# Optimization experiments

Hardware: AMD Instinct MI355X
Metric: run time of the kernel (lower is better)

## Reference

```python
import jax, jax.numpy as jnp
import numpy as np

N = 50000
E = 600000
D_IN, D_HID, D_OUT = 128, 128, 64


def gcn_conv(x, edge_index, W, b):
    """PyG GCNConv: add self-loops, symmetric deg^{-1/2} normalization,
    linear transform, scatter-add aggregation, bias."""
    n = x.shape[0]
    loop = jnp.arange(n, dtype=edge_index.dtype)
    src = jnp.concatenate([edge_index[0], loop])
    dst = jnp.concatenate([edge_index[1], loop])
    h = x @ W  # [N, out]
    deg = jax.ops.segment_sum(jnp.ones_like(dst, dtype=h.dtype), dst, num_segments=n)
    dinv = jnp.where(deg > 0, jax.lax.rsqrt(jnp.maximum(deg, 1e-12)), 0.0)
    norm = dinv[src] * dinv[dst]  # [E+N]
    msg = h[src] * norm[:, None]  # gather + scale
    out = jax.ops.segment_sum(msg, dst, num_segments=n)  # scatter-add
    return out + b


def setup_inputs() -> dict:
    key = jax.random.key(0)
    k1, k2, k3, k4 = jax.random.split(key, 4)
    x = jax.random.normal(k1, (N, D_IN), dtype=jnp.float32)
    edge_index = jax.random.randint(k2, (2, E), 0, N, dtype=jnp.int64)
    s1 = (1.0 / np.sqrt(D_IN)).astype(np.float32) if False else np.float32(1.0 / np.sqrt(D_IN))
    s2 = np.float32(1.0 / np.sqrt(D_HID))
    W1 = jax.random.normal(k3, (D_IN, D_HID), dtype=jnp.float32) * s1
    b1 = jnp.zeros((D_HID,), dtype=jnp.float32)
    W2 = jax.random.normal(k4, (D_HID, D_OUT), dtype=jnp.float32) * s2
    b2 = jnp.zeros((D_OUT,), dtype=jnp.float32)
    return {"x": x, "edge_index": edge_index, "W1": W1, "b1": b1, "W2": W2, "b2": b2}


def reference(x, edge_index, W1, b1, W2, b2):
    # eval mode: dropout p = 0
    h = jax.nn.relu(gcn_conv(x, edge_index, W1, b1))
    return gcn_conv(h, edge_index, W2, b2)
```

## Files before the change

kernel.cpp:

```cpp
#include <hip/hip_runtime.h>
#include <hip/hip_fp16.h>
#include <stdint.h>

#define DIN 128
#define DHID 128
#define DOUT2 64

__device__ __forceinline__ unsigned short f2bf(float f) {
    unsigned u = __float_as_uint(f);
    u += 0x7fffu + ((u >> 16) & 1u);
    return (unsigned short)(u >> 16);
}
__device__ __forceinline__ float bf2f(unsigned short b) {
    return __uint_as_float(((unsigned)b) << 16);
}
__device__ __forceinline__ float bflo(unsigned v) { return __uint_as_float(v << 16); }
__device__ __forceinline__ float bfhi(unsigned v) { return __uint_as_float(v & 0xffff0000u); }
__device__ __forceinline__ unsigned short f2h(float f) {
    return __half_as_ushort(__float2half_rn(f));
}
__device__ __forceinline__ float h2f(unsigned bits) {
    return __half2float(__ushort_as_half((unsigned short)bits));
}

__global__ void detect_i64_kernel(const unsigned* ei, int* flag) {
    int t = threadIdx.x;
    unsigned hi = ei[2 * t + 1];
    unsigned long long vote = __ballot(hi == 0u);
    if (t == 0) *flag = (vote == ~0ull) ? 1 : 0;
}

template <int DO, typename AT>
__device__ __forceinline__ void gemm_block(const AT* __restrict__ A, const float* __restrict__ W,
                                           unsigned short* __restrict__ out, int M, int bx,
                                           float* As, float* Bs) {
    constexpr int CG  = DO / 4;
    constexpr int TYN = 256 / CG;
    constexpr int RM  = 64 / TYN;
    const int tid = threadIdx.x;
    const int row0 = bx * 64;
    const int tx = tid % CG, ty = tid / CG;

    float acc[RM][4];
#pragma unroll
    for (int r = 0; r < RM; r++) acc[r][0] = acc[r][1] = acc[r][2] = acc[r][3] = 0.f;

    for (int k0 = 0; k0 < 128; k0 += 64) {
        for (int idx = tid; idx < 64 * 16; idx += 256) {
            int r = idx >> 4, cc = idx & 15;
            int row = row0 + r;
            float4 v = make_float4(0.f, 0.f, 0.f, 0.f);
            if (row < M) {
                if constexpr (sizeof(AT) == 4) {
                    v = ((const float4*)A)[(size_t)row * 32 + (k0 >> 2) + cc];
                } else {
                    ushort4 u = ((const ushort4*)A)[(size_t)row * 32 + (k0 >> 2) + cc];
                    v = make_float4(bf2f(u.x), bf2f(u.y), bf2f(u.z), bf2f(u.w));
                }
            }
            ((float4*)As)[idx] = v;
        }
        for (int idx = tid; idx < 64 * CG; idx += 256) {
            int r = idx / CG, cc = idx % CG;
            ((float4*)Bs)[idx] = ((const float4*)W)[(size_t)(k0 + r) * CG + cc];
        }
        __syncthreads();
#pragma unroll 8
        for (int k = 0; k < 64; k++) {
            float4 b = ((const float4*)Bs)[k * CG + tx];
#pragma unroll
            for (int r = 0; r < RM; r++) {
                float a = As[(ty * RM + r) * 64 + k];
                acc[r][0] = fmaf(a, b.x, acc[r][0]);
                acc[r][1] = fmaf(a, b.y, acc[r][1]);
                acc[r][2] = fmaf(a, b.z, acc[r][2]);
                acc[r][3] = fmaf(a, b.w, acc[r][3]);
            }
        }
        __syncthreads();
    }
#pragma unroll
    for (int r = 0; r < RM; r++) {
        int row = row0 + ty * RM + r;
        if (row < M) {
            ushort4 v;
            v.x = f2bf(acc[r][0]);
            v.y = f2bf(acc[r][1]);
            v.z = f2bf(acc[r][2]);
            v.w = f2bf(acc[r][3]);
            ((ushort4*)out)[(size_t)row * CG + tx] = v;
        }
    }
}

__global__ __launch_bounds__(256, 2) void fused_gemm_deg_kernel(
    const float* __restrict__ A, const float* __restrict__ W, unsigned short* __restrict__ out,
    int M, int gemmBlocks, const int* ei32, const long long* ei64, const int* flag,
    unsigned* deg, int E) {
    __shared__ float As[64 * 64];
    __shared__ float Bs[64 * DHID];
    if ((int)blockIdx.x < gemmBlocks) {
        gemm_block<DHID, float>(A, W, out, M, blockIdx.x, As, Bs);
    } else {
        int e = (blockIdx.x - gemmBlocks) * 256 + threadIdx.x;
        if (e < E) {
            int mode = *flag;
            int d = mode ? (int)ei64[(size_t)E + e] : ei32[(size_t)E + e];
            atomicAdd(&deg[d], 1u);
        }
    }
}

template <int DO, typename AT>
__global__ __launch_bounds__(256, 2) void gemm_kernel(const AT* __restrict__ A,
                                                      const float* __restrict__ W,
                                                      unsigned short* __restrict__ out, int M) {
    __shared__ float As[64 * 64];
    __shared__ float Bs[64 * DO];
    gemm_block<DO, AT>(A, W, out, M, blockIdx.x, As, Bs);
}

__global__ __launch_bounds__(256) void scan_blocksum_kernel(const unsigned* deg, int* bsum,
                                                            float* dinv, int N) {
    __shared__ int s[256];
    int t = threadIdx.x;
    int base = blockIdx.x * 1024 + t * 4;
    int sum = 0;
    if (base + 3 < N) {
        int4 v = *(const int4*)((const int*)deg + base);
        sum = v.x + v.y + v.z + v.w;
        float4 dv;
        dv.x = rsqrtf((float)(v.x + 1));
        dv.y = rsqrtf((float)(v.y + 1));
        dv.z = rsqrtf((float)(v.z + 1));
        dv.w = rsqrtf((float)(v.w + 1));
        *(float4*)(dinv + base) = dv;
    } else {
        for (int j = 0; j < 4; j++)
            if (base + j < N) {
                int d = (int)deg[base + j];
                sum += d;
                dinv[base + j] = rsqrtf((float)(d + 1));
            }
    }
    s[t] = sum;
    __syncthreads();
    for (int off = 128; off > 0; off >>= 1) {
        if (t < off) s[t] += s[t + off];
        __syncthreads();
    }
    if (t == 0) bsum[blockIdx.x] = s[0];
}

__global__ __launch_bounds__(256) void scan_bsum_kernel(int* bsum, int* row_ptr, int nb, int N) {
    __shared__ int s[256];
    int t = threadIdx.x;
    int v = (t < nb) ? bsum[t] : 0;
    s[t] = v;
    __syncthreads();
    for (int off = 1; off < 256; off <<= 1) {
        int u = (t >= off) ? s[t - off] : 0;
        __syncthreads();
        s[t] += u;
        __syncthreads();
    }
    if (t < nb) bsum[t] = s[t] - v;
    if (t == 255) row_ptr[N] = s[255];
}

__global__ __launch_bounds__(256) void scan_write_kernel(const unsigned* deg, const int* bsum,
                                                         int* row_ptr, int* cursor, int N) {
    __shared__ int s[256];
    int t = threadIdx.x;
    int base = blockIdx.x * 1024 + t * 4;
    int d[4];
    int sum = 0;
#pragma unroll
    for (int j = 0; j < 4; j++) {
        int idx = base + j;
        d[j] = (idx < N) ? (int)deg[idx] : 0;
        sum += d[j];
    }
    s[t] = sum;
    __syncthreads();
    for (int off = 1; off < 256; off <<= 1) {
        int u = (t >= off) ? s[t - off] : 0;
        __syncthreads();
        s[t] += u;
        __syncthreads();
    }
    int run = bsum[blockIdx.x] + s[t] - sum;
#pragma unroll
    for (int j = 0; j < 4; j++) {
        int idx = base + j;
        if (idx < N) {
            row_ptr[idx] = run;
            cursor[idx] = run;
            run += d[j];
        }
    }
}

__global__ void scatter_pack32_kernel(const int* ei32, const long long* ei64, const int* flag,
                                      const float* dinv, int* cursor, unsigned* csr, int E) {
    int e = blockIdx.x * blockDim.x + threadIdx.x;
    if (e >= E) return;
    int mode = *flag;
    int s, d;
    if (mode) {
        s = (int)ei64[e];
        d = (int)ei64[(size_t)E + e];
    } else {
        s = ei32[e];
        d = ei32[(size_t)E + e];
    }
    int pos = atomicAdd(&cursor[d], 1);
    csr[pos] = (unsigned)s | ((unsigned)f2h(dinv[s]) << 16);
}

__global__ void scatter_pack64_kernel(const int* ei32, const long long* ei64, const int* flag,
                                      const float* dinv, int* cursor, unsigned long long* csr,
                                      int E) {
    int e = blockIdx.x * blockDim.x + threadIdx.x;
    if (e >= E) return;
    int mode = *flag;
    int s, d;
    if (mode) {
        s = (int)ei64[e];
        d = (int)ei64[(size_t)E + e];
    } else {
        s = ei32[e];
        d = ei32[(size_t)E + e];
    }
    int pos = atomicAdd(&cursor[d], 1);
    csr[pos] = (unsigned long long)(unsigned)s |
               ((unsigned long long)__float_as_uint(dinv[s]) << 32);
}

__device__ __forceinline__ void unpack(unsigned p, int& s, float& w) {
    s = (int)(p & 0xffffu);
    w = h2f(p >> 16);
}
__device__ __forceinline__ void unpack(unsigned long long p, int& s, float& w) {
    s = (int)(unsigned)(p & 0xffffffffu);
    w = __uint_as_float((unsigned)(p >> 32));
}

template <int D, bool RELU, typename OT, typename CT>
__global__ __launch_bounds__(256) void agg_kernel(const unsigned short* __restrict__ h,
                                                  const CT* __restrict__ csr,
                                                  const int* __restrict__ row_ptr,
                                                  const float* __restrict__ dinv,
                                                  const float* __restrict__ bias,
                                                  OT* __restrict__ out, int N) {
    const int wid = threadIdx.x >> 6;
    const int lane = threadIdx.x & 63;
    const int i = blockIdx.x * 4 + wid;
    if (i >= N) return;
    const float di = dinv[i];
    const int start = row_ptr[i], end = row_ptr[i + 1];

    if constexpr (D == 128) {
        const unsigned* hu = (const unsigned*)h;
        unsigned sv = hu[(size_t)i * 64 + lane];
        float a0 = di * bflo(sv), b0 = di * bfhi(sv);
        float a1 = 0.f, b1 = 0.f;
        int j = start;
        for (; j + 4 <= end; j += 4) {
            CT p0 = csr[j], p1 = csr[j + 1], p2 = csr[j + 2], p3 = csr[j + 3];
            int s0, s1, s2, s3;
            float w0, w1, w2, w3;
            unpack(p0, s0, w0);
            unpack(p1, s1, w1);
            unpack(p2, s2, w2);
            unpack(p3, s3, w3);
            unsigned v0 = hu[(size_t)s0 * 64 + lane];
            unsigned v1 = hu[(size_t)s1 * 64 + lane];
            unsigned v2 = hu[(size_t)s2 * 64 + lane];
            unsigned v3 = hu[(size_t)s3 * 64 + lane];
            a0 = fmaf(w0, bflo(v0), a0);
            b0 = fmaf(w0, bfhi(v0), b0);
            a1 = fmaf(w1, bflo(v1), a1);
            b1 = fmaf(w1, bfhi(v1), b1);
            a0 = fmaf(w2, bflo(v2), a0);
            b0 = fmaf(w2, bfhi(v2), b0);
            a1 = fmaf(w3, bflo(v3), a1);
            b1 = fmaf(w3, bfhi(v3), b1);
        }
        for (; j < end; ++j) {
            int s0;
            float w0;
            unpack(csr[j], s0, w0);
            unsigned v0 = hu[(size_t)s0 * 64 + lane];
            a0 = fmaf(w0, bflo(v0), a0);
            b0 = fmaf(w0, bfhi(v0), b0);
        }
        float2 bv = ((const float2*)bias)[lane];
        float rx = di * (a0 + a1) + bv.x;
        float ry = di * (b0 + b1) + bv.y;
        if (RELU) {
            rx = fmaxf(rx, 0.f);
            ry = fmaxf(ry, 0.f);
        }
        if constexpr (sizeof(OT) == 2) {
            unsigned pv = (unsigned)f2bf(rx) | ((unsigned)f2bf(ry) << 16);
            ((unsigned*)out)[(size_t)i * 64 + lane] = pv;
        } else {
            ((float2*)out)[(size_t)i * 64 + lane] = make_float2(rx, ry);
        }
    } else {
        float a0 = di * bf2f(h[(size_t)i * 64 + lane]);
        float a1 = 0.f;
        int j = start;
        for (; j + 4 <= end; j += 4) {
            CT p0 = csr[j], p1 = csr[j + 1], p2 = csr[j + 2], p3 = csr[j + 3];
            int s0, s1, s2, s3;
            float w0, w1, w2, w3;
            unpack(p0, s0, w0);
            unpack(p1, s1, w1);
            unpack(p2, s2, w2);
            unpack(p3, s3, w3);
            float v0 = bf2f(h[(size_t)s0 * 64 + lane]);
            float v1 = bf2f(h[(size_t)s1 * 64 + lane]);
            float v2 = bf2f(h[(size_t)s2 * 64 + lane]);
            float v3 = bf2f(h[(size_t)s3 * 64 + lane]);
            a0 = fmaf(w0, v0, a0);
            a1 = fmaf(w1, v1, a1);
            a0 = fmaf(w2, v2, a0);
            a1 = fmaf(w3, v3, a1);
        }
        for (; j < end; ++j) {
            int s0;
            float w0;
            unpack(csr[j], s0, w0);
            a0 = fmaf(w0, bf2f(h[(size_t)s0 * 64 + lane]), a0);
        }
        float r = di * (a0 + a1) + bias[lane];
        if (RELU) r = fmaxf(r, 0.f);
        if constexpr (sizeof(OT) == 2) {
            out[(size_t)i * 64 + lane] = (OT)f2bf(r);
        } else {
            out[(size_t)i * 64 + lane] = r;
        }
    }
}

extern "C" void kernel_launch(void* const* d_in, const int* in_sizes, int n_in,
                              void* d_out, int out_size, void* d_ws, size_t ws_size,
                              hipStream_t stream) {
    const float* x  = (const float*)d_in[0];
    const void*  ei = d_in[1];
    const float* W1 = (const float*)d_in[2];
    const float* b1 = (const float*)d_in[3];
    const float* W2 = (const float*)d_in[4];
    const float* b2 = (const float*)d_in[5];
    float* out = (float*)d_out;

    const int N = in_sizes[0] / DIN;
    const int E = in_sizes[1] / 2;

    char* ws = (char*)d_ws;
    size_t off = 0;
    auto alloc = [&](size_t bytes) -> void* {
        void* p = ws + off;
        off += (bytes + 255) & ~(size_t)255;
        return p;
    };
    unsigned*       deg  = (unsigned*)alloc((size_t)N * 4);
    float*          dinv = (float*)alloc((size_t)N * 4);
    int*            rowp = (int*)alloc((size_t)(N + 1) * 4);
    int*            curs = (int*)alloc((size_t)N * 4);
    int*            flag = (int*)alloc(256);
    int*            bsum = (int*)alloc(1024 * 4);
    void*           csr  = alloc((size_t)E * 8);
    unsigned short* h1   = (unsigned short*)alloc((size_t)N * DHID * 2);
    unsigned short* o1   = (unsigned short*)alloc((size_t)N * DHID * 2);
    unsigned short* h2   = h1;

    const int nb = (N + 1023) / 1024;
    const int gemmBlocks = (N + 63) / 64;
    const int degBlocks = (E + 255) / 256;

    hipMemsetAsync(deg, 0, (size_t)N * 4, stream);
    detect_i64_kernel<<<1, 64, 0, stream>>>((const unsigned*)ei, flag);
    fused_gemm_deg_kernel<<<gemmBlocks + degBlocks, 256, 0, stream>>>(
        x, W1, h1, N, gemmBlocks, (const int*)ei, (const long long*)ei, flag, deg, E);
    scan_blocksum_kernel<<<nb, 256, 0, stream>>>(deg, bsum, dinv, N);
    scan_bsum_kernel<<<1, 256, 0, stream>>>(bsum, rowp, nb, N);
    scan_write_kernel<<<nb, 256, 0, stream>>>(deg, bsum, rowp, curs, N);

    if (N <= 65535) {
        unsigned* csr32 = (unsigned*)csr;
        scatter_pack32_kernel<<<degBlocks, 256, 0, stream>>>(
            (const int*)ei, (const long long*)ei, flag, dinv, curs, csr32, E);
        agg_kernel<DHID, true, unsigned short, unsigned><<<(N + 3) / 4, 256, 0, stream>>>(
            h1, csr32, rowp, dinv, b1, o1, N);
        gemm_kernel<DOUT2, unsigned short><<<gemmBlocks, 256, 0, stream>>>(o1, W2, h2, N);
        agg_kernel<DOUT2, false, float, unsigned><<<(N + 3) / 4, 256, 0, stream>>>(
            h2, csr32, rowp, dinv, b2, out, N);
    } else {
        unsigned long long* csr64 = (unsigned long long*)csr;
        scatter_pack64_kernel<<<degBlocks, 256, 0, stream>>>(
            (const int*)ei, (const long long*)ei, flag, dinv, curs, csr64, E);
        agg_kernel<DHID, true, unsigned short, unsigned long long><<<(N + 3) / 4, 256, 0,
                                                                     stream>>>(h1, csr64, rowp,
                                                                               dinv, b1, o1, N);
        gemm_kernel<DOUT2, unsigned short><<<gemmBlocks, 256, 0, stream>>>(o1, W2, h2, N);
        agg_kernel<DOUT2, false, float, unsigned long long><<<(N + 3) / 4, 256, 0, stream>>>(
            h2, csr64, rowp, dinv, b2, out, N);
    }
}
```

Measured before the change: 243.2 us.

## Replace FP32 SIMT GEMMs with bf16 MFMA kernels and split degree counting

Both dense transforms (x@W1 and o1@W2) now run on matrix cores via mfma_f32_16x16x32_bf16. Inputs and weights are converted to bf16 and staged in padded LDS tiles, with W transposed. The degree atomic counting moves out of the fused GEMM kernel into its own launch. This is meant to cut the FP32 FMA cost of the GEMMs, at the price of bf16 rounding of x and W1 and one extra kernel launch.

After: 243.3 us. Within noise of the previous version (+0.1%).

```diff
diff --git a/kernel.cpp b/kernel.cpp
--- a/kernel.cpp
+++ b/kernel.cpp
@@ -5,6 +5,9 @@
 #define DIN 128
 #define DHID 128
 #define DOUT2 64
+
+typedef __attribute__((ext_vector_type(8))) short short8v;
+typedef __attribute__((ext_vector_type(4))) float f32x4;
 
 __device__ __forceinline__ unsigned short f2bf(float f) {
     unsigned u = __float_as_uint(f);
@@ -30,94 +33,87 @@
     if (t == 0) *flag = (vote == ~0ull) ? 1 : 0;
 }
 
+__global__ void deg_count_kernel(const int* ei32, const long long* ei64, const int* flag,
+                                 unsigned* deg, int E) {
+    int e = blockIdx.x * blockDim.x + threadIdx.x;
+    if (e >= E) return;
+    int mode = *flag;
+    int d = mode ? (int)ei64[(size_t)E + e] : ei32[(size_t)E + e];
+    atomicAdd(&deg[d], 1u);
+}
+
 template <int DO, typename AT>
-__device__ __forceinline__ void gemm_block(const AT* __restrict__ A, const float* __restrict__ W,
-                                           unsigned short* __restrict__ out, int M, int bx,
-                                           float* As, float* Bs) {
-    constexpr int CG  = DO / 4;
-    constexpr int TYN = 256 / CG;
-    constexpr int RM  = 64 / TYN;
+__global__ __launch_bounds__(256) void gemm_mfma_kernel(const AT* __restrict__ A,
+                                                        const float* __restrict__ W,
+                                                        unsigned short* __restrict__ out,
+                                                        int M) {
+    constexpr int NT = DO / 16;
+    __shared__ unsigned short As[64 * 136];
+    __shared__ unsigned short Wt[DO * 136];
     const int tid = threadIdx.x;
-    const int row0 = bx * 64;
-    const int tx = tid % CG, ty = tid / CG;
-
-    float acc[RM][4];
-#pragma unroll
-    for (int r = 0; r < RM; r++) acc[r][0] = acc[r][1] = acc[r][2] = acc[r][3] = 0.f;
-
-    for (int k0 = 0; k0 < 128; k0 += 64) {
+    const int row0 = blockIdx.x * 64;
+
+    for (int idx = tid; idx < 128 * (DO / 4); idx += 256) {
+        int k = idx / (DO / 4);
+        int n4 = (idx % (DO / 4)) * 4;
+        float4 w = ((const float4*)W)[idx];
+        Wt[(n4 + 0) * 136 + k] = f2bf(w.x);
+        Wt[(n4 + 1) * 136 + k] = f2bf(w.y);
+        Wt[(n4 + 2) * 136 + k] = f2bf(w.z);
+        Wt[(n4 + 3) * 136 + k] = f2bf(w.w);
+    }
+    if constexpr (sizeof(AT) == 4) {
+        for (int idx = tid; idx < 64 * 32; idx += 256) {
+            int r = idx >> 5, c4 = idx & 31;
+            int row = row0 + r;
+            ushort4 o = {0, 0, 0, 0};
+            if (row < M) {
+                float4 v = ((const float4*)A)[(size_t)row * 32 + c4];
+                o.x = f2bf(v.x);
+                o.y = f2bf(v.y);
+                o.z = f2bf(v.z);
+                o.w = f2bf(v.w);
+            }
+            *(ushort4*)&As[r * 136 + c4 * 4] = o;
+        }
+    } else {
         for (int idx = tid; idx < 64 * 16; idx += 256) {
-            int r = idx >> 4, cc = idx & 15;
+            int r = idx >> 4, c8 = idx & 15;
             int row = row0 + r;
-            float4 v = make_float4(0.f, 0.f, 0.f, 0.f);
-            if (row < M) {
-                if constexpr (sizeof(AT) == 4) {
-                    v = ((const float4*)A)[(size_t)row * 32 + (k0 >> 2) + cc];
-                } else {
-                    ushort4 u = ((const ushort4*)A)[(size_t)row * 32 + (k0 >> 2) + cc];
-                    v = make_float4(bf2f(u.x), bf2f(u.y), bf2f(u.z), bf2f(u.w));
-                }
-            }
-            ((float4*)As)[idx] = v;
-        }
-        for (int idx = tid; idx < 64 * CG; idx += 256) {
-            int r = idx / CG, cc = idx % CG;
-            ((float4*)Bs)[idx] = ((const float4*)W)[(size_t)(k0 + r) * CG + cc];
-        }
-        __syncthreads();
-#pragma unroll 8
-        for (int k = 0; k < 64; k++) {
-            float4 b = ((const float4*)Bs)[k * CG + tx];
-#pragma unroll
-            for (int r = 0; r < RM; r++) {
-                float a = As[(ty * RM + r) * 64 + k];
-                acc[r][0] = fmaf(a, b.x, acc[r][0]);
-                acc[r][1] = fmaf(a, b.y, acc[r][1]);
-                acc[r][2] = fmaf(a, b.z, acc[r][2]);
-                acc[r][3] = fmaf(a, b.w, acc[r][3]);
-            }
-        }
-        __syncthreads();
-    }
-#pragma unroll
-    for (int r = 0; r < RM; r++) {
-        int row = row0 + ty * RM + r;
-        if (row < M) {
-            ushort4 v;
-            v.x = f2bf(acc[r][0]);
-            v.y = f2bf(acc[r][1]);
-            v.z = f2bf(acc[r][2]);
-            v.w = f2bf(acc[r][3]);
-            ((ushort4*)out)[(size_t)row * CG + tx] = v;
-        }
-    }
-}
-
-__global__ __launch_bounds__(256, 2) void fused_gemm_deg_kernel(
-    const float* __restrict__ A, const float* __restrict__ W, unsigned short* __restrict__ out,
-    int M, int gemmBlocks, const int* ei32, const long long* ei64, const int* flag,
-    unsigned* deg, int E) {
-    __shared__ float As[64 * 64];
-    __shared__ float Bs[64 * DHID];
-    if ((int)blockIdx.x < gemmBlocks) {
-        gemm_block<DHID, float>(A, W, out, M, blockIdx.x, As, Bs);
-    } else {
-        int e = (blockIdx.x - gemmBlocks) * 256 + threadIdx.x;
-        if (e < E) {
-            int mode = *flag;
-            int d = mode ? (int)ei64[(size_t)E + e] : ei32[(size_t)E + e];
-            atomicAdd(&deg[d], 1u);
-        }
-    }
-}
-
-template <int DO, typename AT>
-__global__ __launch_bounds__(256, 2) void gemm_kernel(const AT* __restrict__ A,
-                                                      const float* __restrict__ W,
-                                                      unsigned short* __restrict__ out, int M) {
-    __shared__ float As[64 * 64];
-    __shared__ float Bs[64 * DO];
-    gemm_block<DO, AT>(A, W, out, M, blockIdx.x, As, Bs);
+            uint4 v = {0u, 0u, 0u, 0u};
+            if (row < M) v = ((const uint4*)A)[(size_t)row * 16 + c8];
+            *(uint4*)&As[r * 136 + c8 * 8] = v;
+        }
+    }
+    __syncthreads();
+
+    const int wid = tid >> 6, lane = tid & 63;
+    const int r16 = lane & 15, g = lane >> 4;
+    f32x4 acc[NT];
+#pragma unroll
+    for (int n = 0; n < NT; n++) acc[n] = (f32x4){0.f, 0.f, 0.f, 0.f};
+
+    const unsigned short* a_base = &As[(wid * 16 + r16) * 136 + g * 8];
+    const unsigned short* b_base = &Wt[r16 * 136 + g * 8];
+#pragma unroll
+    for (int kk = 0; kk < 4; kk++) {
+        short8v a = *(const short8v*)(a_base + kk * 32);
+#pragma unroll
+        for (int n = 0; n < NT; n++) {
+            short8v b = *(const short8v*)(b_base + n * 16 * 136 + kk * 32);
+            acc[n] = __builtin_amdgcn_mfma_f32_16x16x32_bf16(a, b, acc[n], 0, 0, 0);
+        }
+    }
+
+    const int rbase = row0 + wid * 16 + g * 4;
+#pragma unroll
+    for (int n = 0; n < NT; n++) {
+#pragma unroll
+        for (int q = 0; q < 4; q++) {
+            int row = rbase + q;
+            if (row < M) out[(size_t)row * DO + n * 16 + r16] = f2bf(acc[n][q]);
+        }
+    }
 }
 
 __global__ __launch_bounds__(256) void scan_blocksum_kernel(const unsigned* deg, int* bsum,
@@ -383,8 +379,9 @@
 
     hipMemsetAsync(deg, 0, (size_t)N * 4, stream);
     detect_i64_kernel<<<1, 64, 0, stream>>>((const unsigned*)ei, flag);
-    fused_gemm_deg_kernel<<<gemmBlocks + degBlocks, 256, 0, stream>>>(
-        x, W1, h1, N, gemmBlocks, (const int*)ei, (const long long*)ei, flag, deg, E);
+    deg_count_kernel<<<degBlocks, 256, 0, stream>>>((const int*)ei, (const long long*)ei, flag,
+                                                    deg, E);
+    gemm_mfma_kernel<DHID, float><<<gemmBlocks, 256, 0, stream>>>(x, W1, h1, N);
     scan_blocksum_kernel<<<nb, 256, 0, stream>>>(deg, bsum, dinv, N);
     scan_bsum_kernel<<<1, 256, 0, stream>>>(bsum, rowp, nb, N);
     scan_write_kernel<<<nb, 256, 0, stream>>>(deg, bsum, rowp, curs, N);
@@ -395,7 +392,7 @@
             (const int*)ei, (const long long*)ei, flag, dinv, curs, csr32, E);
         agg_kernel<DHID, true, unsigned short, unsigned><<<(N + 3) / 4, 256, 0, stream>>>(
             h1, csr32, rowp, dinv, b1, o1, N);
-        gemm_kernel<DOUT2, unsigned short><<<gemmBlocks, 256, 0, stream>>>(o1, W2, h2, N);
+        gemm_mfma_kernel<DOUT2, unsigned short><<<gemmBlocks, 256, 0, stream>>>(o1, W2, h2, N);
         agg_kernel<DOUT2, false, float, unsigned><<<(N + 3) / 4, 256, 0, stream>>>(
             h2, csr32, rowp, dinv, b2, out, N);
     } else {
@@ -405,7 +402,7 @@
         agg_kernel<DHID, true, unsigned short, unsigned long long><<<(N + 3) / 4, 256, 0,
                                                                      stream>>>(h1, csr64, rowp,
                                                                                dinv, b1, o1, N);
-        gemm_kernel<DOUT2, unsigned short><<<gemmBlocks, 256, 0, stream>>>(o1, W2, h2, N);
+        gemm_mfma_kernel<DOUT2, unsigned short><<<gemmBlocks, 256, 0, stream>>>(o1, W2, h2, N);
         agg_kernel<DOUT2, false, float, unsigned long long><<<(N + 3) / 4, 256, 0, stream>>>(
             h2, csr64, rowp, dinv, b2, out, N);
     }
```
